# Kernel optimization log

Hardware: AMD Instinct MI355X
Metric: run time of the kernel (lower is better)

Reference implementation:

```python
import jax, jax.numpy as jnp
import numpy as np

B, N, C_IN, C_OUT, CHEB_K, EMBED = 64, 2048, 64, 64, 3, 16

def setup_inputs() -> dict:
    key = jax.random.key(0)
    k1, k2, k3, k4 = jax.random.split(key, 4)
    x = jax.random.normal(k1, (B, N, C_IN), dtype=jnp.float32)
    node_embedding = jax.random.normal(k2, (N, EMBED), dtype=jnp.float32)
    weights_pool = jax.random.normal(k3, (EMBED, CHEB_K, C_IN, C_OUT), dtype=jnp.float32) * 0.1
    bias_pool = jax.random.normal(k4, (EMBED, C_OUT), dtype=jnp.float32) * 0.1
    return {"x": x, "node_embedding": node_embedding,
            "weights_pool": weights_pool, "bias_pool": bias_pool}

def reference(x, node_embedding, weights_pool, bias_pool):
    cheb_k = weights_pool.shape[1]
    n = node_embedding.shape[0]
    # adaptive adjacency: softmax over rows of relu(E @ E^T)
    support = jax.nn.softmax(jax.nn.relu(node_embedding @ node_embedding.T), axis=1)
    # Chebyshev recursion: T0 = I, T1 = support, Tk = 2*support@Tk-1 - Tk-2
    supports = [jnp.eye(n, dtype=support.dtype), support]
    for _ in range(2, cheb_k):
        supports.append(2.0 * support @ supports[-1] - supports[-2])
    supports = jnp.stack(supports, axis=0)  # (K, N, N)
    # per-node weights/bias generated from embedding
    weights = jnp.einsum('nd,dkio->nkio', node_embedding, weights_pool)  # (N,K,Cin,Cout)
    bias = node_embedding @ bias_pool  # (N, Cout)
    # graph conv: gather K-hop features then per-node grouped matmul
    x_g = jnp.einsum('knm,bmc->bnkc', supports, x)  # (B,N,K,Cin)
    x_gconv = jnp.einsum('bnki,nkio->bno', x_g, weights) + bias
    return x_gconv
```

## Files before the change

### kernel.cpp

```cpp
#include <hip/hip_runtime.h>
#include <math.h>

#define NN    2048
#define BATCH 64
#define CIN   64
#define COUT  64
#define EMB   16
#define JDIM  4096
#define WKI   192

typedef __bf16 bf16_t;
typedef __bf16 bf16x8 __attribute__((ext_vector_type(8)));
typedef float  f32x4  __attribute__((ext_vector_type(4)));

#define GLOAD16(gp, lp) __builtin_amdgcn_global_load_lds( \
    (const __attribute__((address_space(1))) void*)(gp),  \
    (__attribute__((address_space(3))) void*)(lp), 16, 0, 0)

static __device__ __forceinline__ unsigned short bfbits(float f) {
    return __builtin_bit_cast(unsigned short, (bf16_t)f);
}

__global__ __launch_bounds__(256) void wgen_kernel(
    const float* __restrict__ E, const float* __restrict__ wp,
    bf16_t* __restrict__ Wt) {
    __shared__ float sE[32][16];
    const int n0 = blockIdx.y * 32;
    const int t  = threadIdx.x;
    const int oki0 = blockIdx.x * 1024 + 4 * t;
    const int o  = oki0 / WKI, r0 = oki0 % WKI;

    if (t < 128) {
        const int node = t >> 2, q = t & 3;
        *reinterpret_cast<float4*>(&sE[node][q * 4]) =
            *reinterpret_cast<const float4*>(E + (size_t)(n0 + node) * EMB + q * 4);
    }

    float w[4][EMB];
#pragma unroll
    for (int d = 0; d < EMB; ++d)
#pragma unroll
        for (int j = 0; j < 4; ++j)
            w[j][d] = wp[(size_t)(d * WKI + r0 + j) * 64 + o];

    __syncthreads();

#pragma unroll 2
    for (int nn = 0; nn < 32; ++nn) {
        float4 e0 = *reinterpret_cast<const float4*>(&sE[nn][0]);
        float4 e1 = *reinterpret_cast<const float4*>(&sE[nn][4]);
        float4 e2 = *reinterpret_cast<const float4*>(&sE[nn][8]);
        float4 e3 = *reinterpret_cast<const float4*>(&sE[nn][12]);
        float en[EMB] = {e0.x,e0.y,e0.z,e0.w, e1.x,e1.y,e1.z,e1.w,
                         e2.x,e2.y,e2.z,e2.w, e3.x,e3.y,e3.z,e3.w};
        float a[4] = {};
#pragma unroll
        for (int d = 0; d < EMB; ++d) {
#pragma unroll
            for (int j = 0; j < 4; ++j) a[j] += en[d] * w[j][d];
        }
        ushort4 pk;
        pk.x = bfbits(a[0]); pk.y = bfbits(a[1]);
        pk.z = bfbits(a[2]); pk.w = bfbits(a[3]);
        *reinterpret_cast<ushort4*>(Wt + (size_t)(n0 + nn) * 12288 + oki0) = pk;
    }
}

__global__ __launch_bounds__(256) void y0_kernel(const float* __restrict__ x,
                                                 bf16_t* __restrict__ Y0) {
    __shared__ float tile[64][65];
    const int n0 = blockIdx.x * 64, b = blockIdx.y, tid = threadIdx.x;
    const int c = tid & 63, nn0 = tid >> 6;
    const float* src = x + ((size_t)b * NN + n0) * CIN + c;
#pragma unroll
    for (int p = 0; p < 16; ++p) {
        int nn = nn0 + p * 4;
        tile[nn][c] = src[(size_t)nn * CIN];
    }
    __syncthreads();
    const int cc = tid >> 2, q = tid & 3;
    bf16_t* dst = Y0 + (size_t)(b * 64 + cc) * NN + n0 + q * 16;
#pragma unroll
    for (int s4 = 0; s4 < 4; ++s4) {
        ushort4 pk;
        pk.x = bfbits(tile[q * 16 + s4 * 4 + 0][cc]);
        pk.y = bfbits(tile[q * 16 + s4 * 4 + 1][cc]);
        pk.z = bfbits(tile[q * 16 + s4 * 4 + 2][cc]);
        pk.w = bfbits(tile[q * 16 + s4 * 4 + 3][cc]);
        *reinterpret_cast<ushort4*>(dst + s4 * 4) = pk;
    }
}

__global__ __launch_bounds__(256) void support_kernel(
    const float* __restrict__ E, bf16_t* __restrict__ Sb) {
    const int n = blockIdx.x, tid = threadIdx.x;
    __shared__ float vals[NN];
    __shared__ float red[4];

    float en[EMB];
#pragma unroll
    for (int d = 0; d < EMB; ++d) en[d] = E[n * EMB + d];

    float lmax = -1e30f;
    for (int m = tid; m < NN; m += 256) {
        const float4* em = reinterpret_cast<const float4*>(E + m * EMB);
        float dot = 0.f;
#pragma unroll
        for (int q = 0; q < EMB / 4; ++q) {
            float4 v = em[q];
            dot += en[q*4+0]*v.x + en[q*4+1]*v.y + en[q*4+2]*v.z + en[q*4+3]*v.w;
        }
        float r = fmaxf(dot, 0.f);
        vals[m] = r;
        lmax = fmaxf(lmax, r);
    }
#pragma unroll
    for (int off = 32; off > 0; off >>= 1)
        lmax = fmaxf(lmax, __shfl_down(lmax, off, 64));
    if ((tid & 63) == 0) red[tid >> 6] = lmax;
    __syncthreads();
    const float gmax = fmaxf(fmaxf(red[0], red[1]), fmaxf(red[2], red[3]));
    __syncthreads();

    float lsum = 0.f;
    for (int m = tid; m < NN; m += 256) {
        float e = expf(vals[m] - gmax);
        vals[m] = e;
        lsum += e;
    }
#pragma unroll
    for (int off = 32; off > 0; off >>= 1)
        lsum += __shfl_down(lsum, off, 64);
    if ((tid & 63) == 0) red[tid >> 6] = lsum;
    __syncthreads();
    const float inv = 1.f / (red[0] + red[1] + red[2] + red[3]);

    for (int m = tid; m < NN; m += 256)
        Sb[(size_t)n * NN + m] = (bf16_t)(vals[m] * inv);
}

template<int MODE>
__global__ __launch_bounds__(256) void gemm_bt(
    const bf16_t* __restrict__ A, const bf16_t* __restrict__ Bt,
    bf16_t* __restrict__ Cj, bf16_t* __restrict__ GT) {
    __shared__ bf16_t smem[128 * 136];
    bf16_t* As = smem;
    bf16_t* Bs = smem + 4096;
    bf16_t* T  = smem;
    const int tid  = threadIdx.x;
    const int wave = tid >> 6, lane = tid & 63;
    const int pBlk = blockIdx.x * 128;
    const int mBlk = blockIdx.y * 128;
    const int K = NN;

    const bf16_t* aSrc = A  + (size_t)(mBlk + wave * 32 + (lane >> 2)) * K + (lane & 3) * 8;
    const bf16_t* bSrc = Bt + (size_t)(pBlk + wave * 32 + (lane >> 2)) * K + (lane & 3) * 8;
    bf16_t* aDst = As + wave * 1024;
    bf16_t* bDst = Bs + wave * 1024;

    f32x4 acc[4][4] = {};
    const int wr = wave >> 1, wc = wave & 1;
    const int lrow = lane & 15, lk = (lane >> 4) * 8;

    for (int k0 = 0; k0 < K; k0 += 32) {
        GLOAD16(aSrc + k0,                  aDst);
        GLOAD16(aSrc + k0 + (size_t)16 * K, aDst + 512);
        GLOAD16(bSrc + k0,                  bDst);
        GLOAD16(bSrc + k0 + (size_t)16 * K, bDst + 512);
        __syncthreads();

        bf16x8 af[4], bb[4];
#pragma unroll
        for (int mf = 0; mf < 4; ++mf)
            af[mf] = *reinterpret_cast<const bf16x8*>(
                &As[(wr * 64 + mf * 16 + lrow) * 32 + lk]);
#pragma unroll
        for (int nf = 0; nf < 4; ++nf)
            bb[nf] = *reinterpret_cast<const bf16x8*>(
                &Bs[(wc * 64 + nf * 16 + lrow) * 32 + lk]);
#pragma unroll
        for (int mf = 0; mf < 4; ++mf)
#pragma unroll
            for (int nf = 0; nf < 4; ++nf)
                acc[mf][nf] = __builtin_amdgcn_mfma_f32_16x16x32_bf16(
                    af[mf], bb[nf], acc[mf][nf], 0, 0, 0);
        __syncthreads();
    }

    const int orow = (lane >> 4) * 4, ocol = lane & 15;
    if (MODE == 0) {
#pragma unroll
        for (int mf = 0; mf < 4; ++mf)
#pragma unroll
            for (int nf = 0; nf < 4; ++nf)
#pragma unroll
                for (int r = 0; r < 4; ++r) {
                    size_t row = (size_t)(mBlk + wr * 64 + mf * 16 + orow + r);
                    size_t col = (size_t)(pBlk + wc * 64 + nf * 16 + ocol);
                    Cj[row * NN + col] = (bf16_t)acc[mf][nf][r];
                }
    }
    const float scale = (MODE == 1) ? 2.f : 1.f;
#pragma unroll
    for (int mf = 0; mf < 4; ++mf)
#pragma unroll
        for (int nf = 0; nf < 4; ++nf)
#pragma unroll
            for (int r = 0; r < 4; ++r) {
                int trow = wr * 64 + mf * 16 + orow + r;
                int tcol = wc * 64 + nf * 16 + ocol;
                T[(size_t)tcol * 136 + trow] = (bf16_t)(scale * acc[mf][nf][r]);
            }
    __syncthreads();
    {
        const int row = tid >> 1, half = tid & 1;
        const bf16_t* src = T + (size_t)row * 136 + half * 64;
        bf16_t* dst = GT + (size_t)(pBlk + row) * JDIM + mBlk + half * 64;
#pragma unroll
        for (int s = 0; s < 8; ++s)
            *reinterpret_cast<uint4*>(dst + s * 8) =
                *reinterpret_cast<const uint4*>(src + s * 8);
    }
}

__global__ __launch_bounds__(256) void gconv_kernel(
    const float* __restrict__ x,   const float* __restrict__ E,
    const float* __restrict__ bp,  const bf16_t* __restrict__ G1T,
    const bf16_t* __restrict__ G2T, const bf16_t* __restrict__ Wt,
    float* __restrict__ out) {
    __shared__ bf16_t g[64][200];
    const int n = blockIdx.x;
    const int tid = threadIdx.x, wave = tid >> 6, lane = tid & 63;
    const int lrow = lane & 15, lk = (lane >> 4) * 8;
    const int o = wave * 16 + lrow;

    const bf16_t* wtn = Wt + (size_t)n * 12288 + (size_t)o * WKI;
    bf16x8 bb[6];
#pragma unroll
    for (int ks = 0; ks < 6; ++ks)
        bb[ks] = *reinterpret_cast<const bf16x8*>(wtn + ks * 32 + lk);
    float bo = 0.f;
    {
        const float* en = E + (size_t)n * EMB;
#pragma unroll
        for (int d = 0; d < EMB; ++d) bo += en[d] * bp[d * COUT + o];
    }

#pragma unroll
    for (int p = 0; p < 2; ++p) {
        int idx = p * 256 + tid;
        int b = idx >> 3, ic = (idx & 7) * 8;
        const float4* xs = reinterpret_cast<const float4*>(
            x + ((size_t)b * NN + n) * CIN + ic);
        float4 x0 = xs[0], x1 = xs[1];
        uint4 g1v = *reinterpret_cast<const uint4*>(G1T + (size_t)n * JDIM + idx * 8);
        uint4 g2v = *reinterpret_cast<const uint4*>(G2T + (size_t)n * JDIM + idx * 8);
        float xv[8] = {x0.x, x0.y, x0.z, x0.w, x1.x, x1.y, x1.z, x1.w};
        const bf16_t* g2p = reinterpret_cast<const bf16_t*>(&g2v);
        ushort4 g0b[2], g2b[2];
#pragma unroll
        for (int e = 0; e < 8; ++e) {
            ((unsigned short*)g0b)[e] = bfbits(xv[e]);
            ((unsigned short*)g2b)[e] = bfbits((float)g2p[e] - xv[e]);
        }
        *reinterpret_cast<uint4*>(&g[b][ic])       = *reinterpret_cast<uint4*>(g0b);
        *reinterpret_cast<uint4*>(&g[b][64 + ic])  = g1v;
        *reinterpret_cast<uint4*>(&g[b][128 + ic]) = *reinterpret_cast<uint4*>(g2b);
    }
    __syncthreads();

    f32x4 acc[4] = {};
#pragma unroll
    for (int ks = 0; ks < 6; ++ks)
#pragma unroll
        for (int mf = 0; mf < 4; ++mf) {
            bf16x8 af = *reinterpret_cast<const bf16x8*>(&g[mf * 16 + lrow][ks * 32 + lk]);
            acc[mf] = __builtin_amdgcn_mfma_f32_16x16x32_bf16(af, bb[ks], acc[mf], 0, 0, 0);
        }
#pragma unroll
    for (int mf = 0; mf < 4; ++mf)
#pragma unroll
        for (int r = 0; r < 4; ++r) {
            int b = mf * 16 + (lane >> 4) * 4 + r;
            out[((size_t)b * NN + n) * COUT + o] = acc[mf][r] + bo;
        }
}

extern "C" void kernel_launch(void* const* d_in, const int* in_sizes, int n_in,
                              void* d_out, int out_size, void* d_ws, size_t ws_size,
                              hipStream_t stream) {
    const float* x  = (const float*)d_in[0];
    const float* E  = (const float*)d_in[1];
    const float* wp = (const float*)d_in[2];
    const float* bp = (const float*)d_in[3];
    float* out = (float*)d_out;

    bf16_t* ws = (bf16_t*)d_ws;
    bf16_t* Wt  = ws;
    bf16_t* Sb  = Wt + (size_t)NN * 12288;
    bf16_t* Y0  = Sb + (size_t)NN * NN;
    bf16_t* Y1  = Y0 + (size_t)JDIM * NN;
    bf16_t* G1T = Y1 + (size_t)JDIM * NN;
    bf16_t* G2T = Y0;

    wgen_kernel<<<dim3(12288 / 1024, NN / 32), 256, 0, stream>>>(E, wp, Wt);
    support_kernel<<<NN, 256, 0, stream>>>(E, Sb);
    y0_kernel<<<dim3(NN / 64, BATCH), 256, 0, stream>>>(x, Y0);

    dim3 ggrid(NN / 128, JDIM / 128);
    gemm_bt<0><<<ggrid, 256, 0, stream>>>(Y0, Sb, Y1, G1T);
    gemm_bt<1><<<ggrid, 256, 0, stream>>>(Y1, Sb, nullptr, G2T);

    gconv_kernel<<<NN, 256, 0, stream>>>(x, E, bp, G1T, G2T, Wt, out);
}
```

Measured before the change: 279.7 us.

## Merge wgen, support and y0 into one prelude launch; add nontemporal stores

Combines the three independent preprocessing kernels (weight generation, softmax support, x transpose) into a single launch that dispatches on block index, so their work runs concurrently and two launch gaps disappear. It also marks the Wt stores, the Wt loads in gconv and the output stores as nontemporal, so streaming data does not pollute the cache. The merged kernel's shared memory is now the size of the largest branch, which could lower occupancy for the smaller branches.

```diff
diff --git a/kernel.cpp b/kernel.cpp
--- a/kernel.cpp
+++ b/kernel.cpp
@@ -12,6 +12,8 @@
 typedef __bf16 bf16_t;
 typedef __bf16 bf16x8 __attribute__((ext_vector_type(8)));
 typedef float  f32x4  __attribute__((ext_vector_type(4)));
+typedef unsigned int u32x2 __attribute__((ext_vector_type(2)));
+typedef unsigned int u32x4 __attribute__((ext_vector_type(4)));
 
 #define GLOAD16(gp, lp) __builtin_amdgcn_global_load_lds( \
     (const __attribute__((address_space(1))) void*)(gp),  \
@@ -21,122 +23,122 @@
     return __builtin_bit_cast(unsigned short, (bf16_t)f);
 }
 
-__global__ __launch_bounds__(256) void wgen_kernel(
-    const float* __restrict__ E, const float* __restrict__ wp,
-    bf16_t* __restrict__ Wt) {
-    __shared__ float sE[32][16];
-    const int n0 = blockIdx.y * 32;
-    const int t  = threadIdx.x;
-    const int oki0 = blockIdx.x * 1024 + 4 * t;
-    const int o  = oki0 / WKI, r0 = oki0 % WKI;
-
-    if (t < 128) {
-        const int node = t >> 2, q = t & 3;
-        *reinterpret_cast<float4*>(&sE[node][q * 4]) =
-            *reinterpret_cast<const float4*>(E + (size_t)(n0 + node) * EMB + q * 4);
-    }
-
-    float w[4][EMB];
-#pragma unroll
-    for (int d = 0; d < EMB; ++d)
-#pragma unroll
-        for (int j = 0; j < 4; ++j)
-            w[j][d] = wp[(size_t)(d * WKI + r0 + j) * 64 + o];
-
-    __syncthreads();
+__global__ __launch_bounds__(256) void prelude_kernel(
+    const float* __restrict__ x,  const float* __restrict__ E,
+    const float* __restrict__ wp, bf16_t* __restrict__ Y0,
+    bf16_t* __restrict__ Sb,      bf16_t* __restrict__ Wt) {
+    __shared__ float smem[64 * 65];
+    const int bid = blockIdx.x;
+    const int tid = threadIdx.x;
+
+    if (bid < 768) {
+        float (*sE)[16] = reinterpret_cast<float(*)[16]>(smem);
+        const int n0   = (bid / 12) * 32;
+        const int oki0 = (bid % 12) * 1024 + 4 * tid;
+        const int o = oki0 / WKI, r0 = oki0 % WKI;
+
+        if (tid < 128) {
+            const int node = tid >> 2, q = tid & 3;
+            *reinterpret_cast<float4*>(&sE[node][q * 4]) =
+                *reinterpret_cast<const float4*>(E + (size_t)(n0 + node) * EMB + q * 4);
+        }
+        float w[4][EMB];
+#pragma unroll
+        for (int d = 0; d < EMB; ++d)
+#pragma unroll
+            for (int j = 0; j < 4; ++j)
+                w[j][d] = wp[(size_t)(d * WKI + r0 + j) * 64 + o];
+        __syncthreads();
 
 #pragma unroll 2
-    for (int nn = 0; nn < 32; ++nn) {
-        float4 e0 = *reinterpret_cast<const float4*>(&sE[nn][0]);
-        float4 e1 = *reinterpret_cast<const float4*>(&sE[nn][4]);
-        float4 e2 = *reinterpret_cast<const float4*>(&sE[nn][8]);
-        float4 e3 = *reinterpret_cast<const float4*>(&sE[nn][12]);
-        float en[EMB] = {e0.x,e0.y,e0.z,e0.w, e1.x,e1.y,e1.z,e1.w,
-                         e2.x,e2.y,e2.z,e2.w, e3.x,e3.y,e3.z,e3.w};
-        float a[4] = {};
-#pragma unroll
-        for (int d = 0; d < EMB; ++d) {
-#pragma unroll
-            for (int j = 0; j < 4; ++j) a[j] += en[d] * w[j][d];
-        }
-        ushort4 pk;
-        pk.x = bfbits(a[0]); pk.y = bfbits(a[1]);
-        pk.z = bfbits(a[2]); pk.w = bfbits(a[3]);
-        *reinterpret_cast<ushort4*>(Wt + (size_t)(n0 + nn) * 12288 + oki0) = pk;
-    }
-}
-
-__global__ __launch_bounds__(256) void y0_kernel(const float* __restrict__ x,
-                                                 bf16_t* __restrict__ Y0) {
-    __shared__ float tile[64][65];
-    const int n0 = blockIdx.x * 64, b = blockIdx.y, tid = threadIdx.x;
-    const int c = tid & 63, nn0 = tid >> 6;
-    const float* src = x + ((size_t)b * NN + n0) * CIN + c;
-#pragma unroll
-    for (int p = 0; p < 16; ++p) {
-        int nn = nn0 + p * 4;
-        tile[nn][c] = src[(size_t)nn * CIN];
-    }
-    __syncthreads();
-    const int cc = tid >> 2, q = tid & 3;
-    bf16_t* dst = Y0 + (size_t)(b * 64 + cc) * NN + n0 + q * 16;
-#pragma unroll
-    for (int s4 = 0; s4 < 4; ++s4) {
-        ushort4 pk;
-        pk.x = bfbits(tile[q * 16 + s4 * 4 + 0][cc]);
-        pk.y = bfbits(tile[q * 16 + s4 * 4 + 1][cc]);
-        pk.z = bfbits(tile[q * 16 + s4 * 4 + 2][cc]);
-        pk.w = bfbits(tile[q * 16 + s4 * 4 + 3][cc]);
-        *reinterpret_cast<ushort4*>(dst + s4 * 4) = pk;
-    }
-}
-
-__global__ __launch_bounds__(256) void support_kernel(
-    const float* __restrict__ E, bf16_t* __restrict__ Sb) {
-    const int n = blockIdx.x, tid = threadIdx.x;
-    __shared__ float vals[NN];
-    __shared__ float red[4];
-
-    float en[EMB];
-#pragma unroll
-    for (int d = 0; d < EMB; ++d) en[d] = E[n * EMB + d];
-
-    float lmax = -1e30f;
-    for (int m = tid; m < NN; m += 256) {
-        const float4* em = reinterpret_cast<const float4*>(E + m * EMB);
-        float dot = 0.f;
-#pragma unroll
-        for (int q = 0; q < EMB / 4; ++q) {
-            float4 v = em[q];
-            dot += en[q*4+0]*v.x + en[q*4+1]*v.y + en[q*4+2]*v.z + en[q*4+3]*v.w;
-        }
-        float r = fmaxf(dot, 0.f);
-        vals[m] = r;
-        lmax = fmaxf(lmax, r);
-    }
-#pragma unroll
-    for (int off = 32; off > 0; off >>= 1)
-        lmax = fmaxf(lmax, __shfl_down(lmax, off, 64));
-    if ((tid & 63) == 0) red[tid >> 6] = lmax;
-    __syncthreads();
-    const float gmax = fmaxf(fmaxf(red[0], red[1]), fmaxf(red[2], red[3]));
-    __syncthreads();
-
-    float lsum = 0.f;
-    for (int m = tid; m < NN; m += 256) {
-        float e = expf(vals[m] - gmax);
-        vals[m] = e;
-        lsum += e;
-    }
-#pragma unroll
-    for (int off = 32; off > 0; off >>= 1)
-        lsum += __shfl_down(lsum, off, 64);
-    if ((tid & 63) == 0) red[tid >> 6] = lsum;
-    __syncthreads();
-    const float inv = 1.f / (red[0] + red[1] + red[2] + red[3]);
-
-    for (int m = tid; m < NN; m += 256)
-        Sb[(size_t)n * NN + m] = (bf16_t)(vals[m] * inv);
+        for (int nn = 0; nn < 32; ++nn) {
+            float4 e0 = *reinterpret_cast<const float4*>(&sE[nn][0]);
+            float4 e1 = *reinterpret_cast<const float4*>(&sE[nn][4]);
+            float4 e2 = *reinterpret_cast<const float4*>(&sE[nn][8]);
+            float4 e3 = *reinterpret_cast<const float4*>(&sE[nn][12]);
+            float en[EMB] = {e0.x,e0.y,e0.z,e0.w, e1.x,e1.y,e1.z,e1.w,
+                             e2.x,e2.y,e2.z,e2.w, e3.x,e3.y,e3.z,e3.w};
+            float a[4] = {};
+#pragma unroll
+            for (int d = 0; d < EMB; ++d)
+#pragma unroll
+                for (int j = 0; j < 4; ++j) a[j] += en[d] * w[j][d];
+            ushort4 pk;
+            pk.x = bfbits(a[0]); pk.y = bfbits(a[1]);
+            pk.z = bfbits(a[2]); pk.w = bfbits(a[3]);
+            __builtin_nontemporal_store(
+                __builtin_bit_cast(u32x2, pk),
+                reinterpret_cast<u32x2*>(Wt + (size_t)(n0 + nn) * 12288 + oki0));
+        }
+    } else if (bid < 2816) {
+        float* vals = smem;
+        float* red  = smem + 2048;
+        const int n = bid - 768;
+
+        float en[EMB];
+#pragma unroll
+        for (int d = 0; d < EMB; ++d) en[d] = E[n * EMB + d];
+
+        float lmax = -1e30f;
+        for (int m = tid; m < NN; m += 256) {
+            const float4* em = reinterpret_cast<const float4*>(E + m * EMB);
+            float dot = 0.f;
+#pragma unroll
+            for (int q = 0; q < EMB / 4; ++q) {
+                float4 v = em[q];
+                dot += en[q*4+0]*v.x + en[q*4+1]*v.y + en[q*4+2]*v.z + en[q*4+3]*v.w;
+            }
+            float r = fmaxf(dot, 0.f);
+            vals[m] = r;
+            lmax = fmaxf(lmax, r);
+        }
+#pragma unroll
+        for (int off = 32; off > 0; off >>= 1)
+            lmax = fmaxf(lmax, __shfl_down(lmax, off, 64));
+        if ((tid & 63) == 0) red[tid >> 6] = lmax;
+        __syncthreads();
+        const float gmax = fmaxf(fmaxf(red[0], red[1]), fmaxf(red[2], red[3]));
+        __syncthreads();
+
+        float lsum = 0.f;
+        for (int m = tid; m < NN; m += 256) {
+            float e = expf(vals[m] - gmax);
+            vals[m] = e;
+            lsum += e;
+        }
+#pragma unroll
+        for (int off = 32; off > 0; off >>= 1)
+            lsum += __shfl_down(lsum, off, 64);
+        if ((tid & 63) == 0) red[tid >> 6] = lsum;
+        __syncthreads();
+        const float inv = 1.f / (red[0] + red[1] + red[2] + red[3]);
+
+        for (int m = tid; m < NN; m += 256)
+            Sb[(size_t)n * NN + m] = (bf16_t)(vals[m] * inv);
+    } else {
+        float (*tile)[65] = reinterpret_cast<float(*)[65]>(smem);
+        const int yb = bid - 2816;
+        const int n0 = (yb & 31) * 64, b = yb >> 5;
+        const int c = tid & 63, nn0 = tid >> 6;
+        const float* src = x + ((size_t)b * NN + n0) * CIN + c;
+#pragma unroll
+        for (int p = 0; p < 16; ++p) {
+            int nn = nn0 + p * 4;
+            tile[nn][c] = src[(size_t)nn * CIN];
+        }
+        __syncthreads();
+        const int cc = tid >> 2, q = tid & 3;
+        bf16_t* dst = Y0 + (size_t)(b * 64 + cc) * NN + n0 + q * 16;
+#pragma unroll
+        for (int s4 = 0; s4 < 4; ++s4) {
+            ushort4 pk;
+            pk.x = bfbits(tile[q * 16 + s4 * 4 + 0][cc]);
+            pk.y = bfbits(tile[q * 16 + s4 * 4 + 1][cc]);
+            pk.z = bfbits(tile[q * 16 + s4 * 4 + 2][cc]);
+            pk.w = bfbits(tile[q * 16 + s4 * 4 + 3][cc]);
+            *reinterpret_cast<ushort4*>(dst + s4 * 4) = pk;
+        }
+    }
 }
 
 template<int MODE>
@@ -238,7 +240,8 @@
     bf16x8 bb[6];
 #pragma unroll
     for (int ks = 0; ks < 6; ++ks)
-        bb[ks] = *reinterpret_cast<const bf16x8*>(wtn + ks * 32 + lk);
+        bb[ks] = __builtin_bit_cast(bf16x8, __builtin_nontemporal_load(
+            reinterpret_cast<const u32x4*>(wtn + ks * 32 + lk)));
     float bo = 0.f;
     {
         const float* en = E + (size_t)n * EMB;
@@ -282,7 +285,8 @@
 #pragma unroll
         for (int r = 0; r < 4; ++r) {
             int b = mf * 16 + (lane >> 4) * 4 + r;
-            out[((size_t)b * NN + n) * COUT + o] = acc[mf][r] + bo;
+            __builtin_nontemporal_store(acc[mf][r] + bo,
+                &out[((size_t)b * NN + n) * COUT + o]);
         }
 }
 
@@ -303,9 +307,7 @@
     bf16_t* G1T = Y1 + (size_t)JDIM * NN;
     bf16_t* G2T = Y0;
 
-    wgen_kernel<<<dim3(12288 / 1024, NN / 32), 256, 0, stream>>>(E, wp, Wt);
-    support_kernel<<<NN, 256, 0, stream>>>(E, Sb);
-    y0_kernel<<<dim3(NN / 64, BATCH), 256, 0, stream>>>(x, Y0);
+    prelude_kernel<<<768 + 2048 + 2048, 256, 0, stream>>>(x, E, wp, Y0, Sb, Wt);
 
     dim3 ggrid(NN / 128, JDIM / 128);
     gemm_bt<0><<<ggrid, 256, 0, stream>>>(Y0, Sb, Y1, G1T);
```

New measurement: 264.1 us. 5.6% less time.
